# Performance work log

Hardware: AMD Instinct MI355X
Metric: run time of the kernel (lower is better)

Reference implementation:

```python
import jax, jax.numpy as jnp
import numpy as np

NUM_NODES = 100000
NUM_EDGES = 1600000
D = 128

def sage_conv(x, src, dst, Wl, bl, Wr):
    # PyG SAGEConv (mean aggr): out = lin_l(mean_{j->i} x_j) + lin_r(x_i)
    msgs = x[src]                                            # [E, D] gather
    agg = jax.ops.segment_sum(msgs, dst, num_segments=x.shape[0])  # [N, D]
    deg = jax.ops.segment_sum(jnp.ones((src.shape[0],), x.dtype), dst,
                              num_segments=x.shape[0])       # [N]
    mean = agg / jnp.maximum(deg, 1.0)[:, None]
    return mean @ Wl.T + bl + x @ Wr.T

def setup_inputs() -> dict:
    key = jax.random.key(0)
    ks = jax.random.split(key, 16)
    s = 1.0 / np.sqrt(D)
    inp = {
        'x': jax.random.randint(ks[0], (NUM_NODES, 1), 0, NUM_NODES),
        'edge_index': jax.random.randint(ks[1], (2, NUM_EDGES), 0, NUM_NODES),
        'batch': jnp.zeros((NUM_NODES,), dtype=jnp.int64),
        'item_emb': jax.random.normal(ks[2], (NUM_NODES, D), jnp.float32),
        'edge_emb': jax.random.normal(ks[3], (NUM_EDGES, D), jnp.float32),
        'Wl1': jax.random.uniform(ks[4], (D, D), jnp.float32, -s, s),
        'bl1': jnp.zeros((D,), jnp.float32),
        'Wr1': jax.random.uniform(ks[5], (D, D), jnp.float32, -s, s),
        'Wl2': jax.random.uniform(ks[6], (D, D), jnp.float32, -s, s),
        'bl2': jnp.zeros((D,), jnp.float32),
        'Wr2': jax.random.uniform(ks[7], (D, D), jnp.float32, -s, s),
        'Wl3': jax.random.uniform(ks[8], (D, D), jnp.float32, -s, s),
        'bl3': jnp.zeros((D,), jnp.float32),
        'Wr3': jax.random.uniform(ks[9], (D, D), jnp.float32, -s, s),
        'W_lin1': jax.random.uniform(ks[10], (D, D), jnp.float32, -s, s),
        'b_lin1': jnp.zeros((D,), jnp.float32),
        'W_lin2': jax.random.uniform(ks[11], (D, D), jnp.float32, -s, s),
        'b_lin2': jnp.zeros((D,), jnp.float32),
    }
    return inp

def reference(x, edge_index, batch, item_emb, edge_emb,
              Wl1, bl1, Wr1, Wl2, bl2, Wr2, Wl3, bl3, Wr3,
              W_lin1, b_lin1, W_lin2, b_lin2):
    src, dst = edge_index[0], edge_index[1]
    h = item_emb[x[:, 0]]                      # embedding lookup + squeeze(1) -> [N, D]
    e = edge_emb                               # edge_embedding(arange(E)) == full table
    h = jax.nn.relu(sage_conv(h, src, dst, Wl1, bl1, Wr1))
    h = jax.nn.relu(sage_conv(h, src, dst, Wl2, bl2, Wr2))
    h = jax.nn.relu(sage_conv(h, src, dst, Wl3, bl3, Wr3))
    h = jax.nn.relu(h @ W_lin1.T + b_lin1)     # dropout is identity in eval mode
    e_out = jax.nn.relu(e @ W_lin2.T + b_lin2)
    return h, e_out
```

## Files before the change

kernel.cpp:

```cpp
#include <hip/hip_runtime.h>

#define NN  100000
#define NNP 100096
#define NE  1600000
#define DD  128

typedef __attribute__((ext_vector_type(8))) short bf16x8;
typedef __attribute__((ext_vector_type(4))) float f32x4;

__device__ __forceinline__ float bf2f(unsigned short u){
  union { unsigned int i; float f; } v; v.i = ((unsigned int)u) << 16; return v.f;
}
__device__ __forceinline__ unsigned short f2bf(float f){
  union { float f; unsigned int i; } v; v.f = f;
  unsigned int u = v.i;
  return (unsigned short)((u + 0x7fffu + ((u >> 16) & 1u)) >> 16);
}
__device__ __forceinline__ unsigned int cvt_pk_bf16(float lo, float hi){
  unsigned int r;
  asm("v_cvt_pk_bf16_f32 %0, %1, %2" : "=v"(r) : "v"(lo), "v"(hi));
  return r;
}

struct WPtrs { const float* w[8]; };
__global__ __launch_bounds__(256) void cvt_w_all(WPtrs wp, unsigned short* __restrict__ o){
  int t = blockIdx.x * 256 + threadIdx.x;
  int m = t >> 13, i = t & 8191;
  float2 v = ((const float2*)wp.w[m])[i];
  ((unsigned int*)o)[t] = cvt_pk_bf16(v.x, v.y);
}

__global__ __launch_bounds__(256) void count_deg(const int* __restrict__ dst,
                                                 int* __restrict__ deg, int n){
  int t = blockIdx.x * 256 + threadIdx.x;
  if (t < n) atomicAdd(&deg[dst[t]], 1);
}

#define SCAN_CHUNK 1024
__global__ __launch_bounds__(256) void partial_sums(const int* __restrict__ deg,
                                                    int* __restrict__ partials, int n){
  __shared__ int lds[256];
  int t = threadIdx.x;
  int base = blockIdx.x * SCAN_CHUNK + t * 4;
  int s = 0;
  #pragma unroll
  for (int i = 0; i < 4; ++i){ int idx = base + i; s += (idx < n) ? deg[idx] : 0; }
  lds[t] = s; __syncthreads();
  for (int off = 128; off > 0; off >>= 1){
    if (t < off) lds[t] += lds[t + off];
    __syncthreads();
  }
  if (t == 0) partials[blockIdx.x] = lds[0];
}

__global__ void scan_partials(int* partials, int nb){
  if (threadIdx.x == 0 && blockIdx.x == 0){
    int acc = 0;
    for (int i = 0; i < nb; ++i){ int v = partials[i]; partials[i] = acc; acc += v; }
  }
}

__global__ __launch_bounds__(256) void scan_block(const int* __restrict__ deg,
                                                  const int* __restrict__ partials,
                                                  int* __restrict__ row_start, int n){
  __shared__ int lds[256];
  int t = threadIdx.x;
  int base = blockIdx.x * SCAN_CHUNK + t * 4;
  int v[4]; int s = 0;
  #pragma unroll
  for (int i = 0; i < 4; ++i){ int idx = base + i; v[i] = (idx < n) ? deg[idx] : 0; s += v[i]; }
  lds[t] = s; __syncthreads();
  for (int off = 1; off < 256; off <<= 1){
    int x = (t >= off) ? lds[t - off] : 0;
    __syncthreads();
    lds[t] += x;
    __syncthreads();
  }
  int excl = ((t == 0) ? 0 : lds[t - 1]) + partials[blockIdx.x];
  #pragma unroll
  for (int i = 0; i < 4; ++i){ int idx = base + i; if (idx < n) row_start[idx] = excl; excl += v[i]; }
}

__global__ __launch_bounds__(256) void fill_csr(const int* __restrict__ src,
                                                const int* __restrict__ dst,
                                                const int* __restrict__ row_start,
                                                int* __restrict__ cursor,
                                                int* __restrict__ csr, int n){
  int t = blockIdx.x * 256 + threadIdx.x;
  if (t < n){
    int d = dst[t];
    int pos = atomicAdd(&cursor[d], 1);
    csr[row_start[d] + pos] = src[t];
  }
}

__global__ __launch_bounds__(256) void gather_h0(const int* __restrict__ x,
                                                 const float* __restrict__ emb,
                                                 unsigned short* __restrict__ h, int n){
  int t = blockIdx.x * 256 + threadIdx.x;
  if (t >= n * 64) return;
  int node = t >> 6, p = t & 63;
  int s = x[node];
  float2 v = *(const float2*)(emb + (size_t)s * DD + p * 2);
  ((unsigned int*)h)[t] = cvt_pk_bf16(v.x, v.y);
}

__global__ __launch_bounds__(256) void aggregate2(const unsigned short* __restrict__ h,
                                                  const int* __restrict__ csr,
                                                  const int* __restrict__ row_start,
                                                  const int* __restrict__ deg,
                                                  unsigned short* __restrict__ mean, int n){
  int node = blockIdx.x * 4 + (threadIdx.x >> 6);
  if (node >= n) return;
  int lane = threadIdx.x & 63;
  int st = row_start[node];
  int d = deg[node];
  const unsigned int* hp = (const unsigned int*)h;
  float s0 = 0.f, s1 = 0.f, t0 = 0.f, t1 = 0.f;
  float u0 = 0.f, u1 = 0.f, w0 = 0.f, w1 = 0.f;
  int i = 0;
  for (; i + 4 <= d; i += 4){
    int n0 = csr[st + i], n1 = csr[st + i + 1], n2 = csr[st + i + 2], n3 = csr[st + i + 3];
    unsigned int v0 = hp[(size_t)n0 * 64 + lane];
    unsigned int v1 = hp[(size_t)n1 * 64 + lane];
    unsigned int v2 = hp[(size_t)n2 * 64 + lane];
    unsigned int v3 = hp[(size_t)n3 * 64 + lane];
    s0 += bf2f((unsigned short)(v0 & 0xffffu)); s1 += bf2f((unsigned short)(v0 >> 16));
    t0 += bf2f((unsigned short)(v1 & 0xffffu)); t1 += bf2f((unsigned short)(v1 >> 16));
    u0 += bf2f((unsigned short)(v2 & 0xffffu)); u1 += bf2f((unsigned short)(v2 >> 16));
    w0 += bf2f((unsigned short)(v3 & 0xffffu)); w1 += bf2f((unsigned short)(v3 >> 16));
  }
  for (; i < d; ++i){
    int s = csr[st + i];
    unsigned int v = hp[(size_t)s * 64 + lane];
    s0 += bf2f((unsigned short)(v & 0xffffu)); s1 += bf2f((unsigned short)(v >> 16));
  }
  s0 += t0 + u0 + w0;
  s1 += t1 + u1 + w1;
  float inv = 1.0f / fmaxf((float)d, 1.0f);
  ((unsigned int*)mean)[(size_t)node * 64 + lane] = cvt_pk_bf16(s0 * inv, s1 * inv);
}

__device__ __forceinline__ void stage_mat(const unsigned short* __restrict__ Bg,
                                          unsigned short* sB){
  int t = threadIdx.x;
  #pragma unroll
  for (int it = 0; it < 8; ++it){
    int idx = it * 256 + t;
    int kc = idx >> 7, col = idx & 127;
    uint4 v = *(const uint4*)(Bg + (size_t)col * DD + kc * 8);
    *(uint4*)(sB + (size_t)idx * 8) = v;
  }
}

__global__ __launch_bounds__(256) void gemm_edge2(
    const float* __restrict__ A, const unsigned short* __restrict__ Bg,
    const float* __restrict__ bias, float* __restrict__ out, int ntiles)
{
  __shared__ unsigned short sB[16384];
  stage_mat(Bg, sB);
  __syncthreads();
  int wave = threadIdx.x >> 6, lane = threadIdx.x & 63;
  int lr = lane & 15, lk = lane >> 4;
  float bv[8];
  #pragma unroll
  for (int j = 0; j < 8; ++j) bv[j] = bias[j * 16 + lr];

  for (int tile = blockIdx.x; tile < ntiles; tile += gridDim.x){
    size_t r0 = (size_t)tile * 128 + wave * 32;
    const float* Ap = A + (r0 + lr) * DD + lk * 8;
    bf16x8 a[2][4];
    #pragma unroll
    for (int g = 0; g < 2; ++g){
      #pragma unroll
      for (int ks = 0; ks < 4; ++ks){
        f32x4 a0 = *(const f32x4*)(Ap + (size_t)g * 16 * DD + ks * 32);
        f32x4 a1 = *(const f32x4*)(Ap + (size_t)g * 16 * DD + ks * 32 + 4);
        union { bf16x8 v; unsigned int u[4]; } au;
        au.u[0] = cvt_pk_bf16(a0[0], a0[1]);
        au.u[1] = cvt_pk_bf16(a0[2], a0[3]);
        au.u[2] = cvt_pk_bf16(a1[0], a1[1]);
        au.u[3] = cvt_pk_bf16(a1[2], a1[3]);
        a[g][ks] = au.v;
      }
    }
    f32x4 acc[2][8];
    #pragma unroll
    for (int g = 0; g < 2; ++g)
      #pragma unroll
      for (int j = 0; j < 8; ++j) acc[g][j] = (f32x4){0.f, 0.f, 0.f, 0.f};
    #pragma unroll
    for (int ks = 0; ks < 4; ++ks){
      #pragma unroll
      for (int j = 0; j < 8; ++j){
        bf16x8 b = *(const bf16x8*)(sB + ((ks * 4 + lk) * 128 + j * 16 + lr) * 8);
        acc[0][j] = __builtin_amdgcn_mfma_f32_16x16x32_bf16(a[0][ks], b, acc[0][j], 0, 0, 0);
        acc[1][j] = __builtin_amdgcn_mfma_f32_16x16x32_bf16(a[1][ks], b, acc[1][j], 0, 0, 0);
      }
    }
    #pragma unroll
    for (int g = 0; g < 2; ++g)
      #pragma unroll
      for (int j = 0; j < 8; ++j)
        #pragma unroll
        for (int r = 0; r < 4; ++r){
          size_t row = r0 + g * 16 + lk * 4 + r;
          out[row * DD + j * 16 + lr] = fmaxf(acc[g][j][r] + bv[j], 0.f);
        }
  }
}

template<int DUAL, int OUTF32>
__global__ __launch_bounds__(256) void gemm_node2(
    const unsigned short* __restrict__ A1, const unsigned short* __restrict__ B1g,
    const unsigned short* __restrict__ A2, const unsigned short* __restrict__ B2g,
    const float* __restrict__ bias, void* __restrict__ outp, int M, int ntiles)
{
  __shared__ unsigned short sB[DUAL ? 32768 : 16384];
  stage_mat(B1g, sB);
  if (DUAL) stage_mat(B2g, sB + 16384);
  __syncthreads();
  int wave = threadIdx.x >> 6, lane = threadIdx.x & 63;
  int lr = lane & 15, lk = lane >> 4;
  float bv[8];
  #pragma unroll
  for (int j = 0; j < 8; ++j) bv[j] = bias[j * 16 + lr];

  for (int tile = blockIdx.x; tile < ntiles; tile += gridDim.x){
    size_t r0 = (size_t)tile * 128 + wave * 32;
    f32x4 acc[2][8];
    #pragma unroll
    for (int g = 0; g < 2; ++g)
      #pragma unroll
      for (int j = 0; j < 8; ++j) acc[g][j] = (f32x4){0.f, 0.f, 0.f, 0.f};

    {
      const unsigned short* Ap = A1 + (r0 + lr) * DD + lk * 8;
      bf16x8 a[2][4];
      #pragma unroll
      for (int g = 0; g < 2; ++g)
        #pragma unroll
        for (int ks = 0; ks < 4; ++ks)
          a[g][ks] = *(const bf16x8*)(Ap + (size_t)g * 16 * DD + ks * 32);
      #pragma unroll
      for (int ks = 0; ks < 4; ++ks){
        #pragma unroll
        for (int j = 0; j < 8; ++j){
          bf16x8 b = *(const bf16x8*)(sB + ((ks * 4 + lk) * 128 + j * 16 + lr) * 8);
          acc[0][j] = __builtin_amdgcn_mfma_f32_16x16x32_bf16(a[0][ks], b, acc[0][j], 0, 0, 0);
          acc[1][j] = __builtin_amdgcn_mfma_f32_16x16x32_bf16(a[1][ks], b, acc[1][j], 0, 0, 0);
        }
      }
    }
    if (DUAL){
      const unsigned short* Ap = A2 + (r0 + lr) * DD + lk * 8;
      bf16x8 a[2][4];
      #pragma unroll
      for (int g = 0; g < 2; ++g)
        #pragma unroll
        for (int ks = 0; ks < 4; ++ks)
          a[g][ks] = *(const bf16x8*)(Ap + (size_t)g * 16 * DD + ks * 32);
      #pragma unroll
      for (int ks = 0; ks < 4; ++ks){
        #pragma unroll
        for (int j = 0; j < 8; ++j){
          bf16x8 b = *(const bf16x8*)(sB + 16384 + ((ks * 4 + lk) * 128 + j * 16 + lr) * 8);
          acc[0][j] = __builtin_amdgcn_mfma_f32_16x16x32_bf16(a[0][ks], b, acc[0][j], 0, 0, 0);
          acc[1][j] = __builtin_amdgcn_mfma_f32_16x16x32_bf16(a[1][ks], b, acc[1][j], 0, 0, 0);
        }
      }
    }
    #pragma unroll
    for (int g = 0; g < 2; ++g)
      #pragma unroll
      for (int j = 0; j < 8; ++j)
        #pragma unroll
        for (int r = 0; r < 4; ++r){
          size_t row = r0 + g * 16 + lk * 4 + r;
          float v = fmaxf(acc[g][j][r] + bv[j], 0.f);
          if (OUTF32){
            if (row < (size_t)M) ((float*)outp)[row * DD + j * 16 + lr] = v;
          } else {
            ((unsigned short*)outp)[row * DD + j * 16 + lr] = f2bf(v);
          }
        }
  }
}

extern "C" void kernel_launch(void* const* d_in, const int* in_sizes, int n_in,
                              void* d_out, int out_size, void* d_ws, size_t ws_size,
                              hipStream_t stream)
{
  const int*   x    = (const int*)d_in[0];
  const int*   ei   = (const int*)d_in[1];
  const int*   srcp = ei;
  const int*   dstp = ei + NE;
  const float* item = (const float*)d_in[3];
  const float* eemb = (const float*)d_in[4];
  WPtrs wp;
  wp.w[0] = (const float*)d_in[5];
  wp.w[1] = (const float*)d_in[7];
  wp.w[2] = (const float*)d_in[8];
  wp.w[3] = (const float*)d_in[10];
  wp.w[4] = (const float*)d_in[11];
  wp.w[5] = (const float*)d_in[13];
  wp.w[6] = (const float*)d_in[14];
  wp.w[7] = (const float*)d_in[16];
  const float* bl1 = (const float*)d_in[6];
  const float* bl2 = (const float*)d_in[9];
  const float* bl3 = (const float*)d_in[12];
  const float* bq1 = (const float*)d_in[15];
  const float* bq2 = (const float*)d_in[17];

  char* ws = (char*)d_ws;
  size_t o = 0;
  auto alloc = [&](size_t bytes) -> void* {
    void* p = ws + o;
    o += (bytes + 255) & ~(size_t)255;
    return p;
  };
  unsigned short* wbf      = (unsigned short*)alloc(8 * 16384 * 2);
  int*            deg      = (int*)alloc((size_t)NN * 4);
  int*            cursor   = (int*)alloc((size_t)NN * 4);
  int*            row_st   = (int*)alloc((size_t)NN * 4);
  int*            partials = (int*)alloc(4096);
  int*            csr      = (int*)alloc((size_t)NE * 4);
  unsigned short* mean     = (unsigned short*)alloc((size_t)NNP * DD * 2);
  unsigned short* h_a      = (unsigned short*)alloc((size_t)NNP * DD * 2);
  unsigned short* h_b      = (unsigned short*)alloc((size_t)NNP * DD * 2);

  float* out_h = (float*)d_out;
  float* out_e = out_h + (size_t)NN * DD;

  hipMemsetAsync(deg, 0, (((size_t)NN * 4 + 255) & ~(size_t)255) * 2, stream);

  cvt_w_all<<<256, 256, 0, stream>>>(wp, wbf);

  const int nb = (NN + SCAN_CHUNK - 1) / SCAN_CHUNK;
  count_deg<<<(NE + 255) / 256, 256, 0, stream>>>(dstp, deg, NE);
  partial_sums<<<nb, 256, 0, stream>>>(deg, partials, NN);
  scan_partials<<<1, 64, 0, stream>>>(partials, nb);
  scan_block<<<nb, 256, 0, stream>>>(deg, partials, row_st, NN);
  fill_csr<<<(NE + 255) / 256, 256, 0, stream>>>(srcp, dstp, row_st, cursor, csr, NE);

  gather_h0<<<(NN * 64 + 255) / 256, 256, 0, stream>>>(x, item, h_a, NN);

  const int agg_grid   = (NN + 3) / 4;
  const int node_tiles = NNP / 128;
  const int edge_tiles = NE / 128;

  aggregate2<<<agg_grid, 256, 0, stream>>>(h_a, csr, row_st, deg, mean, NN);
  gemm_node2<1,0><<<node_tiles, 256, 0, stream>>>(mean, wbf + 0*16384, h_a, wbf + 1*16384, bl1, h_b, NN, node_tiles);
  aggregate2<<<agg_grid, 256, 0, stream>>>(h_b, csr, row_st, deg, mean, NN);
  gemm_node2<1,0><<<node_tiles, 256, 0, stream>>>(mean, wbf + 2*16384, h_b, wbf + 3*16384, bl2, h_a, NN, node_tiles);
  aggregate2<<<agg_grid, 256, 0, stream>>>(h_a, csr, row_st, deg, mean, NN);
  gemm_node2<1,0><<<node_tiles, 256, 0, stream>>>(mean, wbf + 4*16384, h_a, wbf + 5*16384, bl3, h_b, NN, node_tiles);

  gemm_node2<0,1><<<node_tiles, 256, 0, stream>>>(h_b, wbf + 6*16384, h_b, wbf + 6*16384, bq1, out_h, NN, node_tiles);

  gemm_edge2<<<2500, 256, 0, stream>>>(eemb, wbf + 7*16384, bq2, out_e, edge_tiles);
}
```

Baseline: 864.6 us.

## Unroll aggregation to 8 gathers and overlap edge GEMM loads with weight staging

The neighbor aggregation now issues 8 independent row gathers per iteration with 8 accumulators, and uses readfirstlane for the row start and degree. The edge GEMM drops its grid-stride loop in favour of one tile per block. It issues its nontemporal A loads before the barrier that follows weight staging, and writes its outputs with nontemporal stores; the fp32 node output also uses nontemporal stores. The goal is more memory-level parallelism and less cache pollution on the streaming traffic. In exchange, each block restages the weights and register pressure rises.

```diff
diff --git a/kernel.cpp b/kernel.cpp
--- a/kernel.cpp
+++ b/kernel.cpp
@@ -105,38 +105,54 @@
   ((unsigned int*)h)[t] = cvt_pk_bf16(v.x, v.y);
 }
 
-__global__ __launch_bounds__(256) void aggregate2(const unsigned short* __restrict__ h,
+__global__ __launch_bounds__(256) void aggregate3(const unsigned short* __restrict__ h,
                                                   const int* __restrict__ csr,
                                                   const int* __restrict__ row_start,
                                                   const int* __restrict__ deg,
                                                   unsigned short* __restrict__ mean, int n){
   int node = blockIdx.x * 4 + (threadIdx.x >> 6);
-  if (node >= n) return;
   int lane = threadIdx.x & 63;
-  int st = row_start[node];
-  int d = deg[node];
+  int st = __builtin_amdgcn_readfirstlane(row_start[node]);
+  int d  = __builtin_amdgcn_readfirstlane(deg[node]);
   const unsigned int* hp = (const unsigned int*)h;
-  float s0 = 0.f, s1 = 0.f, t0 = 0.f, t1 = 0.f;
-  float u0 = 0.f, u1 = 0.f, w0 = 0.f, w1 = 0.f;
+  float a0[8], a1[8];
+  #pragma unroll
+  for (int k = 0; k < 8; ++k){ a0[k] = 0.f; a1[k] = 0.f; }
   int i = 0;
+  for (; i + 8 <= d; i += 8){
+    int idx[8];
+    #pragma unroll
+    for (int k = 0; k < 8; ++k) idx[k] = csr[st + i + k];
+    unsigned int v[8];
+    #pragma unroll
+    for (int k = 0; k < 8; ++k) v[k] = hp[(size_t)idx[k] * 64 + lane];
+    #pragma unroll
+    for (int k = 0; k < 8; ++k){
+      a0[k] += bf2f((unsigned short)(v[k] & 0xffffu));
+      a1[k] += bf2f((unsigned short)(v[k] >> 16));
+    }
+  }
   for (; i + 4 <= d; i += 4){
-    int n0 = csr[st + i], n1 = csr[st + i + 1], n2 = csr[st + i + 2], n3 = csr[st + i + 3];
-    unsigned int v0 = hp[(size_t)n0 * 64 + lane];
-    unsigned int v1 = hp[(size_t)n1 * 64 + lane];
-    unsigned int v2 = hp[(size_t)n2 * 64 + lane];
-    unsigned int v3 = hp[(size_t)n3 * 64 + lane];
-    s0 += bf2f((unsigned short)(v0 & 0xffffu)); s1 += bf2f((unsigned short)(v0 >> 16));
-    t0 += bf2f((unsigned short)(v1 & 0xffffu)); t1 += bf2f((unsigned short)(v1 >> 16));
-    u0 += bf2f((unsigned short)(v2 & 0xffffu)); u1 += bf2f((unsigned short)(v2 >> 16));
-    w0 += bf2f((unsigned short)(v3 & 0xffffu)); w1 += bf2f((unsigned short)(v3 >> 16));
+    int idx[4];
+    #pragma unroll
+    for (int k = 0; k < 4; ++k) idx[k] = csr[st + i + k];
+    unsigned int v[4];
+    #pragma unroll
+    for (int k = 0; k < 4; ++k) v[k] = hp[(size_t)idx[k] * 64 + lane];
+    #pragma unroll
+    for (int k = 0; k < 4; ++k){
+      a0[k] += bf2f((unsigned short)(v[k] & 0xffffu));
+      a1[k] += bf2f((unsigned short)(v[k] >> 16));
+    }
   }
   for (; i < d; ++i){
     int s = csr[st + i];
     unsigned int v = hp[(size_t)s * 64 + lane];
-    s0 += bf2f((unsigned short)(v & 0xffffu)); s1 += bf2f((unsigned short)(v >> 16));
-  }
-  s0 += t0 + u0 + w0;
-  s1 += t1 + u1 + w1;
+    a0[0] += bf2f((unsigned short)(v & 0xffffu));
+    a1[0] += bf2f((unsigned short)(v >> 16));
+  }
+  float s0 = ((a0[0] + a0[1]) + (a0[2] + a0[3])) + ((a0[4] + a0[5]) + (a0[6] + a0[7]));
+  float s1 = ((a1[0] + a1[1]) + (a1[2] + a1[3])) + ((a1[4] + a1[5]) + (a1[6] + a1[7]));
   float inv = 1.0f / fmaxf((float)d, 1.0f);
   ((unsigned int*)mean)[(size_t)node * 64 + lane] = cvt_pk_bf16(s0 * inv, s1 * inv);
 }
@@ -153,61 +169,68 @@
   }
 }
 
-__global__ __launch_bounds__(256) void gemm_edge2(
+__global__ __launch_bounds__(256) void gemm_edge3(
     const float* __restrict__ A, const unsigned short* __restrict__ Bg,
-    const float* __restrict__ bias, float* __restrict__ out, int ntiles)
+    const float* __restrict__ bias, float* __restrict__ out)
 {
   __shared__ unsigned short sB[16384];
   stage_mat(Bg, sB);
-  __syncthreads();
   int wave = threadIdx.x >> 6, lane = threadIdx.x & 63;
   int lr = lane & 15, lk = lane >> 4;
+  size_t r0 = (size_t)blockIdx.x * 128 + (size_t)wave * 32;
+  const float* Ap = A + (r0 + lr) * DD + lk * 8;
+
+  f32x4 raw[2][4][2];
+  #pragma unroll
+  for (int g = 0; g < 2; ++g)
+    #pragma unroll
+    for (int ks = 0; ks < 4; ++ks){
+      raw[g][ks][0] = __builtin_nontemporal_load((const f32x4*)(Ap + (size_t)g * 16 * DD + ks * 32));
+      raw[g][ks][1] = __builtin_nontemporal_load((const f32x4*)(Ap + (size_t)g * 16 * DD + ks * 32 + 4));
+    }
   float bv[8];
   #pragma unroll
   for (int j = 0; j < 8; ++j) bv[j] = bias[j * 16 + lr];
 
-  for (int tile = blockIdx.x; tile < ntiles; tile += gridDim.x){
-    size_t r0 = (size_t)tile * 128 + wave * 32;
-    const float* Ap = A + (r0 + lr) * DD + lk * 8;
-    bf16x8 a[2][4];
-    #pragma unroll
-    for (int g = 0; g < 2; ++g){
-      #pragma unroll
-      for (int ks = 0; ks < 4; ++ks){
-        f32x4 a0 = *(const f32x4*)(Ap + (size_t)g * 16 * DD + ks * 32);
-        f32x4 a1 = *(const f32x4*)(Ap + (size_t)g * 16 * DD + ks * 32 + 4);
-        union { bf16x8 v; unsigned int u[4]; } au;
-        au.u[0] = cvt_pk_bf16(a0[0], a0[1]);
-        au.u[1] = cvt_pk_bf16(a0[2], a0[3]);
-        au.u[2] = cvt_pk_bf16(a1[0], a1[1]);
-        au.u[3] = cvt_pk_bf16(a1[2], a1[3]);
-        a[g][ks] = au.v;
+  __syncthreads();
+
+  bf16x8 a[2][4];
+  #pragma unroll
+  for (int g = 0; g < 2; ++g)
+    #pragma unroll
+    for (int ks = 0; ks < 4; ++ks){
+      union { bf16x8 v; unsigned int u[4]; } au;
+      au.u[0] = cvt_pk_bf16(raw[g][ks][0][0], raw[g][ks][0][1]);
+      au.u[1] = cvt_pk_bf16(raw[g][ks][0][2], raw[g][ks][0][3]);
+      au.u[2] = cvt_pk_bf16(raw[g][ks][1][0], raw[g][ks][1][1]);
+      au.u[3] = cvt_pk_bf16(raw[g][ks][1][2], raw[g][ks][1][3]);
+      a[g][ks] = au.v;
+    }
+
+  f32x4 acc[2][8];
+  #pragma unroll
+  for (int g = 0; g < 2; ++g)
+    #pragma unroll
+    for (int j = 0; j < 8; ++j) acc[g][j] = (f32x4){0.f, 0.f, 0.f, 0.f};
+  #pragma unroll
+  for (int ks = 0; ks < 4; ++ks){
+    #pragma unroll
+    for (int j = 0; j < 8; ++j){
+      bf16x8 b = *(const bf16x8*)(sB + ((ks * 4 + lk) * 128 + j * 16 + lr) * 8);
+      acc[0][j] = __builtin_amdgcn_mfma_f32_16x16x32_bf16(a[0][ks], b, acc[0][j], 0, 0, 0);
+      acc[1][j] = __builtin_amdgcn_mfma_f32_16x16x32_bf16(a[1][ks], b, acc[1][j], 0, 0, 0);
+    }
+  }
+  #pragma unroll
+  for (int g = 0; g < 2; ++g)
+    #pragma unroll
+    for (int j = 0; j < 8; ++j)
+      #pragma unroll
+      for (int r = 0; r < 4; ++r){
+        size_t row = r0 + g * 16 + lk * 4 + r;
+        __builtin_nontemporal_store(fmaxf(acc[g][j][r] + bv[j], 0.f),
+                                    &out[row * DD + j * 16 + lr]);
       }
-    }
-    f32x4 acc[2][8];
-    #pragma unroll
-    for (int g = 0; g < 2; ++g)
-      #pragma unroll
-      for (int j = 0; j < 8; ++j) acc[g][j] = (f32x4){0.f, 0.f, 0.f, 0.f};
-    #pragma unroll
-    for (int ks = 0; ks < 4; ++ks){
-      #pragma unroll
-      for (int j = 0; j < 8; ++j){
-        bf16x8 b = *(const bf16x8*)(sB + ((ks * 4 + lk) * 128 + j * 16 + lr) * 8);
-        acc[0][j] = __builtin_amdgcn_mfma_f32_16x16x32_bf16(a[0][ks], b, acc[0][j], 0, 0, 0);
-        acc[1][j] = __builtin_amdgcn_mfma_f32_16x16x32_bf16(a[1][ks], b, acc[1][j], 0, 0, 0);
-      }
-    }
-    #pragma unroll
-    for (int g = 0; g < 2; ++g)
-      #pragma unroll
-      for (int j = 0; j < 8; ++j)
-        #pragma unroll
-        for (int r = 0; r < 4; ++r){
-          size_t row = r0 + g * 16 + lk * 4 + r;
-          out[row * DD + j * 16 + lr] = fmaxf(acc[g][j][r] + bv[j], 0.f);
-        }
-  }
 }
 
 template<int DUAL, int OUTF32>
@@ -279,7 +302,8 @@
           size_t row = r0 + g * 16 + lk * 4 + r;
           float v = fmaxf(acc[g][j][r] + bv[j], 0.f);
           if (OUTF32){
-            if (row < (size_t)M) ((float*)outp)[row * DD + j * 16 + lr] = v;
+            if (row < (size_t)M)
+              __builtin_nontemporal_store(v, ((float*)outp) + row * DD + j * 16 + lr);
           } else {
             ((unsigned short*)outp)[row * DD + j * 16 + lr] = f2bf(v);
           }
@@ -349,14 +373,14 @@
   const int node_tiles = NNP / 128;
   const int edge_tiles = NE / 128;
 
-  aggregate2<<<agg_grid, 256, 0, stream>>>(h_a, csr, row_st, deg, mean, NN);
+  aggregate3<<<agg_grid, 256, 0, stream>>>(h_a, csr, row_st, deg, mean, NN);
   gemm_node2<1,0><<<node_tiles, 256, 0, stream>>>(mean, wbf + 0*16384, h_a, wbf + 1*16384, bl1, h_b, NN, node_tiles);
-  aggregate2<<<agg_grid, 256, 0, stream>>>(h_b, csr, row_st, deg, mean, NN);
+  aggregate3<<<agg_grid, 256, 0, stream>>>(h_b, csr, row_st, deg, mean, NN);
   gemm_node2<1,0><<<node_tiles, 256, 0, stream>>>(mean, wbf + 2*16384, h_b, wbf + 3*16384, bl2, h_a, NN, node_tiles);
-  aggregate2<<<agg_grid, 256, 0, stream>>>(h_a, csr, row_st, deg, mean, NN);
+  aggregate3<<<agg_grid, 256, 0, stream>>>(h_a, csr, row_st, deg, mean, NN);
   gemm_node2<1,0><<<node_tiles, 256, 0, stream>>>(mean, wbf + 4*16384, h_a, wbf + 5*16384, bl3, h_b, NN, node_tiles);
 
   gemm_node2<0,1><<<node_tiles, 256, 0, stream>>>(h_b, wbf + 6*16384, h_b, wbf + 6*16384, bq1, out_h, NN, node_tiles);
 
-  gemm_edge2<<<2500, 256, 0, stream>>>(eemb, wbf + 7*16384, bq2, out_e, edge_tiles);
-}
+  gemm_edge3<<<edge_tiles, 256, 0, stream>>>(eemb, wbf + 7*16384, bq2, out_e);
+}
```

After: 887.7 us. 2.7% more time.

## Fuse neighbor aggregation with SAGE linear layers and final projection per node tile

Applied to the files above, without the earlier changes.

Each SAGE layer now aggregates neighbor means for a 32-node tile into swizzled shared memory, then applies both Wl and Wr matmuls and ReLU in the same kernel. The last layer also applies the final linear. This removes the mean buffer round trip and separate GEMM launches. The edge GEMM is restructured to one 64-row tile per block with nontemporal loads issued before the weight-staging barrier. Trade-offs: weights are restaged into shared memory for every small block, and the gather loop is unrolled 16-wide, which raises register pressure.

```diff
diff --git a/kernel.cpp b/kernel.cpp
--- a/kernel.cpp
+++ b/kernel.cpp
@@ -105,42 +105,6 @@
   ((unsigned int*)h)[t] = cvt_pk_bf16(v.x, v.y);
 }
 
-__global__ __launch_bounds__(256) void aggregate2(const unsigned short* __restrict__ h,
-                                                  const int* __restrict__ csr,
-                                                  const int* __restrict__ row_start,
-                                                  const int* __restrict__ deg,
-                                                  unsigned short* __restrict__ mean, int n){
-  int node = blockIdx.x * 4 + (threadIdx.x >> 6);
-  if (node >= n) return;
-  int lane = threadIdx.x & 63;
-  int st = row_start[node];
-  int d = deg[node];
-  const unsigned int* hp = (const unsigned int*)h;
-  float s0 = 0.f, s1 = 0.f, t0 = 0.f, t1 = 0.f;
-  float u0 = 0.f, u1 = 0.f, w0 = 0.f, w1 = 0.f;
-  int i = 0;
-  for (; i + 4 <= d; i += 4){
-    int n0 = csr[st + i], n1 = csr[st + i + 1], n2 = csr[st + i + 2], n3 = csr[st + i + 3];
-    unsigned int v0 = hp[(size_t)n0 * 64 + lane];
-    unsigned int v1 = hp[(size_t)n1 * 64 + lane];
-    unsigned int v2 = hp[(size_t)n2 * 64 + lane];
-    unsigned int v3 = hp[(size_t)n3 * 64 + lane];
-    s0 += bf2f((unsigned short)(v0 & 0xffffu)); s1 += bf2f((unsigned short)(v0 >> 16));
-    t0 += bf2f((unsigned short)(v1 & 0xffffu)); t1 += bf2f((unsigned short)(v1 >> 16));
-    u0 += bf2f((unsigned short)(v2 & 0xffffu)); u1 += bf2f((unsigned short)(v2 >> 16));
-    w0 += bf2f((unsigned short)(v3 & 0xffffu)); w1 += bf2f((unsigned short)(v3 >> 16));
-  }
-  for (; i < d; ++i){
-    int s = csr[st + i];
-    unsigned int v = hp[(size_t)s * 64 + lane];
-    s0 += bf2f((unsigned short)(v & 0xffffu)); s1 += bf2f((unsigned short)(v >> 16));
-  }
-  s0 += t0 + u0 + w0;
-  s1 += t1 + u1 + w1;
-  float inv = 1.0f / fmaxf((float)d, 1.0f);
-  ((unsigned int*)mean)[(size_t)node * 64 + lane] = cvt_pk_bf16(s0 * inv, s1 * inv);
-}
-
 __device__ __forceinline__ void stage_mat(const unsigned short* __restrict__ Bg,
                                           unsigned short* sB){
   int t = threadIdx.x;
@@ -153,138 +117,212 @@
   }
 }
 
-__global__ __launch_bounds__(256) void gemm_edge2(
+template<int FINAL>
+__global__ __launch_bounds__(256, 4) void fused_layer(
+    const unsigned short* __restrict__ h_in,
+    const int* __restrict__ csr, const int* __restrict__ row_st,
+    const int* __restrict__ deg,
+    const unsigned short* __restrict__ Wl, const unsigned short* __restrict__ Wr,
+    const float* __restrict__ bl,
+    const unsigned short* __restrict__ Wfin, const float* __restrict__ bfin,
+    unsigned short* __restrict__ h_out, float* __restrict__ f_out)
+{
+  __shared__ unsigned short sW[16384];
+  __shared__ unsigned int   sMean[2048];
+
+  const int tid  = threadIdx.x;
+  const int w    = tid >> 6;
+  const int lane = tid & 63;
+  const int lr   = lane & 15, lk = lane >> 4;
+  const int nodeBase = blockIdx.x * 32;
+
+  stage_mat(Wl, sW);
+
+  const unsigned int* hp = (const unsigned int*)h_in;
+  #pragma unroll 1
+  for (int i = 0; i < 8; ++i){
+    int n  = w * 8 + i;
+    int g  = nodeBase + n;
+    int st = __builtin_amdgcn_readfirstlane(row_st[g]);
+    int d  = __builtin_amdgcn_readfirstlane(deg[g]);
+    float a0 = 0.f, a1 = 0.f, b0 = 0.f, b1 = 0.f;
+    float c0 = 0.f, c1 = 0.f, e0 = 0.f, e1 = 0.f;
+    int k = 0;
+    for (; k + 16 <= d; k += 16){
+      int idx[16];
+      #pragma unroll
+      for (int q = 0; q < 16; ++q) idx[q] = csr[st + k + q];
+      unsigned int vv[16];
+      #pragma unroll
+      for (int q = 0; q < 16; ++q) vv[q] = hp[(size_t)idx[q] * 64 + lane];
+      #pragma unroll
+      for (int q = 0; q < 16; q += 4){
+        a0 += bf2f((unsigned short)(vv[q  ] & 0xffffu)); a1 += bf2f((unsigned short)(vv[q  ] >> 16));
+        b0 += bf2f((unsigned short)(vv[q+1] & 0xffffu)); b1 += bf2f((unsigned short)(vv[q+1] >> 16));
+        c0 += bf2f((unsigned short)(vv[q+2] & 0xffffu)); c1 += bf2f((unsigned short)(vv[q+2] >> 16));
+        e0 += bf2f((unsigned short)(vv[q+3] & 0xffffu)); e1 += bf2f((unsigned short)(vv[q+3] >> 16));
+      }
+    }
+    for (; k + 4 <= d; k += 4){
+      int idx[4];
+      #pragma unroll
+      for (int q = 0; q < 4; ++q) idx[q] = csr[st + k + q];
+      unsigned int vv[4];
+      #pragma unroll
+      for (int q = 0; q < 4; ++q) vv[q] = hp[(size_t)idx[q] * 64 + lane];
+      a0 += bf2f((unsigned short)(vv[0] & 0xffffu)); a1 += bf2f((unsigned short)(vv[0] >> 16));
+      b0 += bf2f((unsigned short)(vv[1] & 0xffffu)); b1 += bf2f((unsigned short)(vv[1] >> 16));
+      c0 += bf2f((unsigned short)(vv[2] & 0xffffu)); c1 += bf2f((unsigned short)(vv[2] >> 16));
+      e0 += bf2f((unsigned short)(vv[3] & 0xffffu)); e1 += bf2f((unsigned short)(vv[3] >> 16));
+    }
+    for (; k < d; ++k){
+      int s = csr[st + k];
+      unsigned int v = hp[(size_t)s * 64 + lane];
+      a0 += bf2f((unsigned short)(v & 0xffffu)); a1 += bf2f((unsigned short)(v >> 16));
+    }
+    float s0 = (a0 + b0) + (c0 + e0);
+    float s1 = (a1 + b1) + (c1 + e1);
+    float inv = 1.0f / fmaxf((float)d, 1.0f);
+    sMean[n * 64 + (lane ^ ((n & 7) << 2))] = cvt_pk_bf16(s0 * inv, s1 * inv);
+  }
+  __syncthreads();
+
+  const int rh = w >> 1, ch = w & 1;
+  float bv[4];
+  #pragma unroll
+  for (int j = 0; j < 4; ++j) bv[j] = bl[ch * 64 + j * 16 + lr];
+
+  f32x4 acc[4];
+  #pragma unroll
+  for (int j = 0; j < 4; ++j) acc[j] = (f32x4){0.f, 0.f, 0.f, 0.f};
+
+  #pragma unroll
+  for (int ks = 0; ks < 4; ++ks){
+    bf16x8 a = *(const bf16x8*)&sMean[(rh * 16 + lr) * 64 + ((ks * 16 + lk * 4) ^ ((lr & 7) << 2))];
+    #pragma unroll
+    for (int j = 0; j < 4; ++j){
+      bf16x8 b = *(const bf16x8*)(sW + (((ks * 4 + lk) * 128) + ch * 64 + j * 16 + lr) * 8);
+      acc[j] = __builtin_amdgcn_mfma_f32_16x16x32_bf16(a, b, acc[j], 0, 0, 0);
+    }
+  }
+  __syncthreads();
+  stage_mat(Wr, sW);
+  __syncthreads();
+
+  {
+    const unsigned short* Ap = h_in + (size_t)(nodeBase + rh * 16 + lr) * DD + lk * 8;
+    #pragma unroll
+    for (int ks = 0; ks < 4; ++ks){
+      bf16x8 a = *(const bf16x8*)(Ap + ks * 32);
+      #pragma unroll
+      for (int j = 0; j < 4; ++j){
+        bf16x8 b = *(const bf16x8*)(sW + (((ks * 4 + lk) * 128) + ch * 64 + j * 16 + lr) * 8);
+        acc[j] = __builtin_amdgcn_mfma_f32_16x16x32_bf16(a, b, acc[j], 0, 0, 0);
+      }
+    }
+  }
+
+  if (!FINAL){
+    #pragma unroll
+    for (int j = 0; j < 4; ++j){
+      int col = ch * 64 + j * 16 + lr;
+      #pragma unroll
+      for (int r = 0; r < 4; ++r){
+        size_t row = (size_t)nodeBase + rh * 16 + lk * 4 + r;
+        h_out[row * DD + col] = f2bf(fmaxf(acc[j][r] + bv[j], 0.f));
+      }
+    }
+    return;
+  }
+
+  __syncthreads();
+  #pragma unroll
+  for (int j = 0; j < 4; ++j){
+    int col = ch * 64 + j * 16 + lr;
+    #pragma unroll
+    for (int r = 0; r < 4; ++r){
+      int n2 = rh * 16 + lk * 4 + r;
+      float v = fmaxf(acc[j][r] + bv[j], 0.f);
+      int uidx = (col >> 1) ^ ((n2 & 7) << 2);
+      ((unsigned short*)sMean)[(n2 * 64 + uidx) * 2 + (col & 1)] = f2bf(v);
+    }
+  }
+  stage_mat(Wfin, sW);
+  __syncthreads();
+
+  float bv2[4];
+  #pragma unroll
+  for (int j = 0; j < 4; ++j) bv2[j] = bfin[ch * 64 + j * 16 + lr];
+  f32x4 acc2[4];
+  #pragma unroll
+  for (int j = 0; j < 4; ++j) acc2[j] = (f32x4){0.f, 0.f, 0.f, 0.f};
+  #pragma unroll
+  for (int ks = 0; ks < 4; ++ks){
+    bf16x8 a = *(const bf16x8*)&sMean[(rh * 16 + lr) * 64 + ((ks * 16 + lk * 4) ^ ((lr & 7) << 2))];
+    #pragma unroll
+    for (int j = 0; j < 4; ++j){
+      bf16x8 b = *(const bf16x8*)(sW + (((ks * 4 + lk) * 128) + ch * 64 + j * 16 + lr) * 8);
+      acc2[j] = __builtin_amdgcn_mfma_f32_16x16x32_bf16(a, b, acc2[j], 0, 0, 0);
+    }
+  }
+  #pragma unroll
+  for (int j = 0; j < 4; ++j){
+    int col = ch * 64 + j * 16 + lr;
+    #pragma unroll
+    for (int r = 0; r < 4; ++r){
+      size_t row = (size_t)nodeBase + rh * 16 + lk * 4 + r;
+      if (row < (size_t)NN)
+        f_out[row * DD + col] = fmaxf(acc2[j][r] + bv2[j], 0.f);
+    }
+  }
+}
+
+__global__ __launch_bounds__(256, 4) void gemm_edge4(
     const float* __restrict__ A, const unsigned short* __restrict__ Bg,
-    const float* __restrict__ bias, float* __restrict__ out, int ntiles)
+    const float* __restrict__ bias, float* __restrict__ out)
 {
   __shared__ unsigned short sB[16384];
   stage_mat(Bg, sB);
-  __syncthreads();
-  int wave = threadIdx.x >> 6, lane = threadIdx.x & 63;
+  int w = threadIdx.x >> 6, lane = threadIdx.x & 63;
   int lr = lane & 15, lk = lane >> 4;
+  size_t r0 = (size_t)blockIdx.x * 64 + (size_t)w * 16;
+  const float* Ap = A + (r0 + lr) * DD + lk * 8;
+
+  f32x4 raw[4][2];
+  #pragma unroll
+  for (int ks = 0; ks < 4; ++ks){
+    raw[ks][0] = __builtin_nontemporal_load((const f32x4*)(Ap + ks * 32));
+    raw[ks][1] = __builtin_nontemporal_load((const f32x4*)(Ap + ks * 32 + 4));
+  }
   float bv[8];
   #pragma unroll
   for (int j = 0; j < 8; ++j) bv[j] = bias[j * 16 + lr];
 
-  for (int tile = blockIdx.x; tile < ntiles; tile += gridDim.x){
-    size_t r0 = (size_t)tile * 128 + wave * 32;
-    const float* Ap = A + (r0 + lr) * DD + lk * 8;
-    bf16x8 a[2][4];
-    #pragma unroll
-    for (int g = 0; g < 2; ++g){
-      #pragma unroll
-      for (int ks = 0; ks < 4; ++ks){
-        f32x4 a0 = *(const f32x4*)(Ap + (size_t)g * 16 * DD + ks * 32);
-        f32x4 a1 = *(const f32x4*)(Ap + (size_t)g * 16 * DD + ks * 32 + 4);
-        union { bf16x8 v; unsigned int u[4]; } au;
-        au.u[0] = cvt_pk_bf16(a0[0], a0[1]);
-        au.u[1] = cvt_pk_bf16(a0[2], a0[3]);
-        au.u[2] = cvt_pk_bf16(a1[0], a1[1]);
-        au.u[3] = cvt_pk_bf16(a1[2], a1[3]);
-        a[g][ks] = au.v;
-      }
-    }
-    f32x4 acc[2][8];
-    #pragma unroll
-    for (int g = 0; g < 2; ++g)
-      #pragma unroll
-      for (int j = 0; j < 8; ++j) acc[g][j] = (f32x4){0.f, 0.f, 0.f, 0.f};
-    #pragma unroll
-    for (int ks = 0; ks < 4; ++ks){
-      #pragma unroll
-      for (int j = 0; j < 8; ++j){
-        bf16x8 b = *(const bf16x8*)(sB + ((ks * 4 + lk) * 128 + j * 16 + lr) * 8);
-        acc[0][j] = __builtin_amdgcn_mfma_f32_16x16x32_bf16(a[0][ks], b, acc[0][j], 0, 0, 0);
-        acc[1][j] = __builtin_amdgcn_mfma_f32_16x16x32_bf16(a[1][ks], b, acc[1][j], 0, 0, 0);
-      }
-    }
-    #pragma unroll
-    for (int g = 0; g < 2; ++g)
-      #pragma unroll
-      for (int j = 0; j < 8; ++j)
-        #pragma unroll
-        for (int r = 0; r < 4; ++r){
-          size_t row = r0 + g * 16 + lk * 4 + r;
-          out[row * DD + j * 16 + lr] = fmaxf(acc[g][j][r] + bv[j], 0.f);
-        }
-  }
-}
-
-template<int DUAL, int OUTF32>
-__global__ __launch_bounds__(256) void gemm_node2(
-    const unsigned short* __restrict__ A1, const unsigned short* __restrict__ B1g,
-    const unsigned short* __restrict__ A2, const unsigned short* __restrict__ B2g,
-    const float* __restrict__ bias, void* __restrict__ outp, int M, int ntiles)
-{
-  __shared__ unsigned short sB[DUAL ? 32768 : 16384];
-  stage_mat(B1g, sB);
-  if (DUAL) stage_mat(B2g, sB + 16384);
-  __syncthreads();
-  int wave = threadIdx.x >> 6, lane = threadIdx.x & 63;
-  int lr = lane & 15, lk = lane >> 4;
-  float bv[8];
-  #pragma unroll
-  for (int j = 0; j < 8; ++j) bv[j] = bias[j * 16 + lr];
-
-  for (int tile = blockIdx.x; tile < ntiles; tile += gridDim.x){
-    size_t r0 = (size_t)tile * 128 + wave * 32;
-    f32x4 acc[2][8];
-    #pragma unroll
-    for (int g = 0; g < 2; ++g)
-      #pragma unroll
-      for (int j = 0; j < 8; ++j) acc[g][j] = (f32x4){0.f, 0.f, 0.f, 0.f};
-
-    {
-      const unsigned short* Ap = A1 + (r0 + lr) * DD + lk * 8;
-      bf16x8 a[2][4];
-      #pragma unroll
-      for (int g = 0; g < 2; ++g)
-        #pragma unroll
-        for (int ks = 0; ks < 4; ++ks)
-          a[g][ks] = *(const bf16x8*)(Ap + (size_t)g * 16 * DD + ks * 32);
-      #pragma unroll
-      for (int ks = 0; ks < 4; ++ks){
-        #pragma unroll
-        for (int j = 0; j < 8; ++j){
-          bf16x8 b = *(const bf16x8*)(sB + ((ks * 4 + lk) * 128 + j * 16 + lr) * 8);
-          acc[0][j] = __builtin_amdgcn_mfma_f32_16x16x32_bf16(a[0][ks], b, acc[0][j], 0, 0, 0);
-          acc[1][j] = __builtin_amdgcn_mfma_f32_16x16x32_bf16(a[1][ks], b, acc[1][j], 0, 0, 0);
-        }
-      }
-    }
-    if (DUAL){
-      const unsigned short* Ap = A2 + (r0 + lr) * DD + lk * 8;
-      bf16x8 a[2][4];
-      #pragma unroll
-      for (int g = 0; g < 2; ++g)
-        #pragma unroll
-        for (int ks = 0; ks < 4; ++ks)
-          a[g][ks] = *(const bf16x8*)(Ap + (size_t)g * 16 * DD + ks * 32);
-      #pragma unroll
-      for (int ks = 0; ks < 4; ++ks){
-        #pragma unroll
-        for (int j = 0; j < 8; ++j){
-          bf16x8 b = *(const bf16x8*)(sB + 16384 + ((ks * 4 + lk) * 128 + j * 16 + lr) * 8);
-          acc[0][j] = __builtin_amdgcn_mfma_f32_16x16x32_bf16(a[0][ks], b, acc[0][j], 0, 0, 0);
-          acc[1][j] = __builtin_amdgcn_mfma_f32_16x16x32_bf16(a[1][ks], b, acc[1][j], 0, 0, 0);
-        }
-      }
-    }
-    #pragma unroll
-    for (int g = 0; g < 2; ++g)
-      #pragma unroll
-      for (int j = 0; j < 8; ++j)
-        #pragma unroll
-        for (int r = 0; r < 4; ++r){
-          size_t row = r0 + g * 16 + lk * 4 + r;
-          float v = fmaxf(acc[g][j][r] + bv[j], 0.f);
-          if (OUTF32){
-            if (row < (size_t)M) ((float*)outp)[row * DD + j * 16 + lr] = v;
-          } else {
-            ((unsigned short*)outp)[row * DD + j * 16 + lr] = f2bf(v);
-          }
-        }
-  }
+  __syncthreads();
+
+  f32x4 acc[8];
+  #pragma unroll
+  for (int j = 0; j < 8; ++j) acc[j] = (f32x4){0.f, 0.f, 0.f, 0.f};
+  #pragma unroll
+  for (int ks = 0; ks < 4; ++ks){
+    union { bf16x8 v; unsigned int u[4]; } au;
+    au.u[0] = cvt_pk_bf16(raw[ks][0][0], raw[ks][0][1]);
+    au.u[1] = cvt_pk_bf16(raw[ks][0][2], raw[ks][0][3]);
+    au.u[2] = cvt_pk_bf16(raw[ks][1][0], raw[ks][1][1]);
+    au.u[3] = cvt_pk_bf16(raw[ks][1][2], raw[ks][1][3]);
+    #pragma unroll
+    for (int j = 0; j < 8; ++j){
+      bf16x8 b = *(const bf16x8*)(sB + (((ks * 4 + lk) * 128) + j * 16 + lr) * 8);
+      acc[j] = __builtin_amdgcn_mfma_f32_16x16x32_bf16(au.v, b, acc[j], 0, 0, 0);
+    }
+  }
+  #pragma unroll
+  for (int j = 0; j < 8; ++j)
+    #pragma unroll
+    for (int r = 0; r < 4; ++r){
+      size_t row = r0 + lk * 4 + r;
+      out[row * DD + j * 16 + lr] = fmaxf(acc[j][r] + bv[j], 0.f);
+    }
 }
 
 extern "C" void kernel_launch(void* const* d_in, const int* in_sizes, int n_in,
@@ -320,19 +358,18 @@
     return p;
   };
   unsigned short* wbf      = (unsigned short*)alloc(8 * 16384 * 2);
-  int*            deg      = (int*)alloc((size_t)NN * 4);
-  int*            cursor   = (int*)alloc((size_t)NN * 4);
-  int*            row_st   = (int*)alloc((size_t)NN * 4);
+  int*            deg      = (int*)alloc((size_t)NNP * 4);
+  int*            cursor   = (int*)alloc((size_t)NNP * 4);
+  int*            row_st   = (int*)alloc((size_t)NNP * 4);
   int*            partials = (int*)alloc(4096);
   int*            csr      = (int*)alloc((size_t)NE * 4);
-  unsigned short* mean     = (unsigned short*)alloc((size_t)NNP * DD * 2);
   unsigned short* h_a      = (unsigned short*)alloc((size_t)NNP * DD * 2);
   unsigned short* h_b      = (unsigned short*)alloc((size_t)NNP * DD * 2);
 
   float* out_h = (float*)d_out;
   float* out_e = out_h + (size_t)NN * DD;
 
-  hipMemsetAsync(deg, 0, (((size_t)NN * 4 + 255) & ~(size_t)255) * 2, stream);
+  hipMemsetAsync(deg, 0, (size_t)NNP * 4 * 3, stream);
 
   cvt_w_all<<<256, 256, 0, stream>>>(wp, wbf);
 
@@ -345,18 +382,14 @@
 
   gather_h0<<<(NN * 64 + 255) / 256, 256, 0, stream>>>(x, item, h_a, NN);
 
-  const int agg_grid   = (NN + 3) / 4;
-  const int node_tiles = NNP / 128;
-  const int edge_tiles = NE / 128;
-
-  aggregate2<<<agg_grid, 256, 0, stream>>>(h_a, csr, row_st, deg, mean, NN);
-  gemm_node2<1,0><<<node_tiles, 256, 0, stream>>>(mean, wbf + 0*16384, h_a, wbf + 1*16384, bl1, h_b, NN, node_tiles);
-  aggregate2<<<agg_grid, 256, 0, stream>>>(h_b, csr, row_st, deg, mean, NN);
-  gemm_node2<1,0><<<node_tiles, 256, 0, stream>>>(mean, wbf + 2*16384, h_b, wbf + 3*16384, bl2, h_a, NN, node_tiles);
-  aggregate2<<<agg_grid, 256, 0, stream>>>(h_a, csr, row_st, deg, mean, NN);
-  gemm_node2<1,0><<<node_tiles, 256, 0, stream>>>(mean, wbf + 4*16384, h_a, wbf + 5*16384, bl3, h_b, NN, node_tiles);
-
-  gemm_node2<0,1><<<node_tiles, 256, 0, stream>>>(h_b, wbf + 6*16384, h_b, wbf + 6*16384, bq1, out_h, NN, node_tiles);
-
-  gemm_edge2<<<2500, 256, 0, stream>>>(eemb, wbf + 7*16384, bq2, out_e, edge_tiles);
-}
+  const int layer_grid = NNP / 32;
+
+  fused_layer<0><<<layer_grid, 256, 0, stream>>>(h_a, csr, row_st, deg,
+      wbf + 0*16384, wbf + 1*16384, bl1, nullptr, nullptr, h_b, nullptr);
+  fused_layer<0><<<layer_grid, 256, 0, stream>>>(h_b, csr, row_st, deg,
+      wbf + 2*16384, wbf + 3*16384, bl2, nullptr, nullptr, h_a, nullptr);
+  fused_layer<1><<<layer_grid, 256, 0, stream>>>(h_a, csr, row_st, deg,
+      wbf + 4*16384, wbf + 5*16384, bl3, wbf + 6*16384, bq1, nullptr, out_h);
+
+  gemm_edge4<<<NE / 64, 256, 0, stream>>>(eemb, wbf + 7*16384, bq2, out_e);
+}
```

After: 951.8 us. 10.1% more time.
